# Optimization experiments

Measured on AMD Instinct MI355X. Metric: run time of the kernel, lower is better.

The kernel has to match this reference:

```python
import jax, jax.numpy as jnp
import numpy as np

B, S, D, V, T, NS, NG = 16, 512, 400, 32000, 8, 30, 3


def setup_inputs() -> dict:
    key = jax.random.key(0)
    ks = jax.random.split(key, 14)
    w = 1.0 / np.sqrt(D)
    return {
        "encoded_hidden": jax.random.normal(ks[0], (1, B, D), jnp.float32) * 0.1,
        "encoded_outputs": jax.random.normal(ks[1], (B, S, D), jnp.float32) * 0.1,
        "story": jax.random.randint(ks[2], (B, S), 0, V),
        "trg_batches": jax.random.randint(ks[3], (B, NS, T), 0, V),
        "shared_emb": jax.random.normal(ks[4], (V, D), jnp.float32) * 0.1,
        "slot_emb": jax.random.normal(ks[5], (1, D), jnp.float32) * 0.1,
        "w_ih": jax.random.normal(ks[6], (3 * D, D), jnp.float32) * w,
        "w_hh": jax.random.normal(ks[7], (3 * D, D), jnp.float32) * w,
        "b_ih": jax.random.normal(ks[8], (3 * D,), jnp.float32) * w,
        "b_hh": jax.random.normal(ks[9], (3 * D,), jnp.float32) * w,
        "w_ratio_w": jax.random.normal(ks[10], (1, 3 * D), jnp.float32) * w,
        "w_ratio_b": jax.random.normal(ks[11], (1,), jnp.float32) * w,
        "w_gate_w": jax.random.normal(ks[12], (NG, D), jnp.float32) * w,
        "w_gate_b": jax.random.normal(ks[13], (NG,), jnp.float32) * w,
        "batch_size": B,
        "max_resp_len": T,
    }


def reference(encoded_hidden, encoded_outputs, story, trg_batches, shared_emb,
              slot_emb, w_ih, w_hh, b_ih, b_hh, w_ratio_w, w_ratio_b,
              w_gate_w, w_gate_b, batch_size, max_resp_len):
    # Original torch code returns inside the slot loop -> only slot 0 is decoded.
    # h0 is re-used as GRU initial state at EVERY step (no carried hidden), and
    # teacher forcing makes each step's input known, so all T steps vectorize.
    h0 = encoded_hidden[0]                         # (B, D)
    Bq, Tq = batch_size, max_resp_len
    Vq = shared_emb.shape[0]

    # decoder inputs: step 0 = slot embedding, steps 1..T-1 = emb(trg[:,0,i-1])
    x0 = jnp.broadcast_to(slot_emb, h0.shape)      # (B, D)
    xt = shared_emb[trg_batches[:, 0, : Tq - 1]]   # (B, T-1, D)
    X = jnp.concatenate([x0[:, None, :], xt], axis=1)  # (B, T, D)

    # GRU cell (torch gate order r, z, n), h0 broadcast over steps
    gi = X @ w_ih.T + b_ih                         # (B, T, 3D)
    gh = h0 @ w_hh.T + b_hh                        # (B, 3D)
    i_r, i_z, i_n = jnp.split(gi, 3, axis=-1)
    h_r, h_z, h_n = jnp.split(gh, 3, axis=-1)
    r = jax.nn.sigmoid(i_r + h_r[:, None, :])
    z = jax.nn.sigmoid(i_z + h_z[:, None, :])
    n = jnp.tanh(i_n + r * h_n[:, None, :])
    h = (1.0 - z) * n + z * h0[:, None, :]         # (B, T, D) decoder_state == hidden

    # attention over history (no length masking: all lens == S)
    scores = jnp.einsum('btd,bsd->bts', h, encoded_outputs)   # (B, T, S)
    probs = jax.nn.softmax(scores, axis=-1)
    # FAITHFUL to original bug: context uses raw scores, not probs
    context = jnp.einsum('bts,bsd->btd', scores, encoded_outputs)

    gate0 = context[:, 0, :] @ w_gate_w.T + w_gate_b          # (B, NG), step i==0

    p_vocab = jax.nn.softmax(h @ shared_emb.T, axis=-1)       # (B, T, V)
    p_gen = jax.nn.sigmoid(
        jnp.concatenate([h, context, X], axis=-1) @ w_ratio_w.T + w_ratio_b
    )                                                         # (B, T, 1)

    # pointer distribution: scatter_add probs onto vocab ids of the story
    p_ctx = jnp.zeros((Bq, Tq, Vq), p_vocab.dtype).at[
        jnp.arange(Bq)[:, None, None],
        jnp.arange(Tq)[None, :, None],
        story[:, None, :],
    ].add(probs)

    p_final = p_gen * p_vocab + (1.0 - p_gen) * p_ctx         # (B, T, V)

    ptr_outputs = jnp.zeros((NS, Bq, Tq, Vq), p_final.dtype).at[0].set(p_final)
    gate_outputs = jnp.zeros((NS, Bq, NG), gate0.dtype).at[0].set(gate0)
    return ptr_outputs, gate_outputs
```

## Files before the change

kernel.cpp:

```cpp
#include <hip/hip_runtime.h>

#define Bq 16
#define Sq 512
#define Dq 400
#define Vq 32000
#define Tq 8
#define NSq 30
#define NGq 3
#define BTq (Bq*Tq)
#define SLICE 4096000
#define PTR_TOTAL (30ull*SLICE)
#define GATE_TOTAL (NSq*Bq*NGq)

#define NCOMPUTE 250
#define NZERO 1813
#define ZPER 16384

__device__ inline float sigmoidf_(float x) { return 1.0f / (1.0f + __expf(-x)); }

__device__ inline float blockReduceSum(float v, float* red) {
    int tid = threadIdx.x;
    #pragma unroll
    for (int o = 32; o > 0; o >>= 1) v += __shfl_down(v, o, 64);
    if ((tid & 63) == 0) red[tid >> 6] = v;
    __syncthreads();
    if (tid == 0) {
        float s = red[0];
        int nw = blockDim.x >> 6;
        for (int i = 1; i < nw; i++) s += red[i];
        red[0] = s;
    }
    __syncthreads();
    float r = red[0];
    __syncthreads();
    return r;
}

__device__ inline float blockReduceMax(float v, float* red) {
    int tid = threadIdx.x;
    #pragma unroll
    for (int o = 32; o > 0; o >>= 1) v = fmaxf(v, __shfl_down(v, o, 64));
    if ((tid & 63) == 0) red[tid >> 6] = v;
    __syncthreads();
    if (tid == 0) {
        float s = red[0];
        int nw = blockDim.x >> 6;
        for (int i = 1; i < nw; i++) s = fmaxf(s, red[i]);
        red[0] = s;
    }
    __syncthreads();
    float r = red[0];
    __syncthreads();
    return r;
}

__global__ __launch_bounds__(256) void k_gates(const float* __restrict__ enc_hidden,
                                               const float* __restrict__ shared_emb,
                                               const float* __restrict__ slot_emb,
                                               const float* __restrict__ w_ih,
                                               const float* __restrict__ w_hh,
                                               const float* __restrict__ b_ih,
                                               const float* __restrict__ b_hh,
                                               const int* __restrict__ trg,
                                               float* __restrict__ gi, float* __restrict__ gh) {
    __shared__ float A[9][Dq];
    __shared__ int toks[8];
    int b = blockIdx.x >> 2, jt = blockIdx.x & 3;
    int tid = threadIdx.x;
    if (tid < 7) toks[tid + 1] = trg[b * (NSq * Tq) + tid];
    __syncthreads();
    for (int idx = tid; idx < 900; idx += 256) {
        int r = idx / 100, q = idx - r * 100;
        const float4* src;
        if (r == 8)      src = (const float4*)(enc_hidden + b * Dq);
        else if (r == 0) src = (const float4*)slot_emb;
        else             src = (const float4*)(shared_emb + (size_t)toks[r] * Dq);
        *(float4*)&A[r][4 * q] = src[q];
    }
    __syncthreads();
    for (int o = tid; o < 2700; o += 256) {
        int r = o / 300, jj = o - r * 300;
        int j = jt * 300 + jj;
        const float* w = (r == 8) ? w_hh : w_ih;
        const float4* w4 = (const float4*)(w + (size_t)j * Dq);
        const float4* a4 = (const float4*)&A[r][0];
        float acc = (r == 8) ? b_hh[j] : b_ih[j];
        #pragma unroll 4
        for (int q = 0; q < Dq / 4; ++q) {
            float4 wv = w4[q], av = a4[q];
            acc += av.x * wv.x + av.y * wv.y + av.z * wv.z + av.w * wv.w;
        }
        if (r == 8) gh[b * 1200 + j] = acc;
        else        gi[(b * 8 + r) * 1200 + j] = acc;
    }
}

__global__ __launch_bounds__(512) void k_attn(const float* __restrict__ gi,
                                              const float* __restrict__ gh,
                                              const float* __restrict__ enc_hidden,
                                              const float* __restrict__ shared_emb,
                                              const float* __restrict__ slot_emb,
                                              const int* __restrict__ trg,
                                              const float* __restrict__ enc_out,
                                              const int* __restrict__ story,
                                              const float* __restrict__ w_ratio_w,
                                              const float* __restrict__ w_ratio_b,
                                              const float* __restrict__ w_gate_w,
                                              const float* __restrict__ w_gate_b,
                                              float* __restrict__ pctx, float* __restrict__ pgen,
                                              float* __restrict__ hT, float* __restrict__ out_gate) {
    __shared__ float h_l[Dq], ctx_l[Dq], x_l[Dq], sc_l[Sq], red[8];
    int bt = blockIdx.x, b = bt >> 3, t = bt & 7;
    int tid = threadIdx.x;
    if (tid < Dq) {
        int d = tid;
        float x = (t == 0) ? slot_emb[d]
                           : shared_emb[(size_t)trg[b * (NSq * Tq) + (t - 1)] * Dq + d];
        float h0 = enc_hidden[b * Dq + d];
        const float* gib = gi + bt * 1200;
        const float* ghb = gh + b * 1200;
        float r_ = sigmoidf_(gib[d] + ghb[d]);
        float z  = sigmoidf_(gib[Dq + d] + ghb[Dq + d]);
        float n  = tanhf(gib[2 * Dq + d] + r_ * ghb[2 * Dq + d]);
        float h  = (1.0f - z) * n + z * h0;
        h_l[d] = h; x_l[d] = x;
        hT[d * BTq + bt] = h;
    }
    __syncthreads();
    {
        const float4* e4 = (const float4*)(enc_out + ((size_t)(b * Sq + tid)) * Dq);
        float acc = 0.0f;
        for (int q = 0; q < Dq / 4; ++q) {
            float4 p = e4[q];
            int k = 4 * q;
            acc += h_l[k]*p.x + h_l[k+1]*p.y + h_l[k+2]*p.z + h_l[k+3]*p.w;
        }
        sc_l[tid] = acc;
    }
    __syncthreads();
    float myv = sc_l[tid];
    float m = blockReduceMax(myv, red);
    float e = __expf(myv - m);
    float ssum = blockReduceSum(e, red);
    atomicAdd(&pctx[(size_t)bt * Vq + story[b * Sq + tid]], e / ssum);
    for (int d = tid; d < Dq; d += 512) {
        float acc = 0.0f;
        #pragma unroll 8
        for (int s = 0; s < Sq; ++s)
            acc += sc_l[s] * enc_out[((size_t)(b * Sq + s)) * Dq + d];
        ctx_l[d] = acc;
    }
    __syncthreads();
    {
        float part = 0.0f;
        for (int i = tid; i < 1200; i += 512) {
            float v = (i < Dq) ? h_l[i] : (i < 2 * Dq ? ctx_l[i - Dq] : x_l[i - 2 * Dq]);
            part += v * w_ratio_w[i];
        }
        float tot = blockReduceSum(part, red);
        if (tid == 0) pgen[bt] = sigmoidf_(tot + w_ratio_b[0]);
    }
    if (t == 0) {
        for (int g = 0; g < NGq; ++g) {
            float part = 0.0f;
            for (int d = tid; d < Dq; d += 512) part += ctx_l[d] * w_gate_w[g * Dq + d];
            float tot = blockReduceSum(part, red);
            if (tid == 0) out_gate[b * NGq + g] = tot + w_gate_b[g];
        }
    }
}

#define TVL 128
#define CKL 40
__global__ __launch_bounds__(256) void k_logits(const float* __restrict__ hT,
                                                const float* __restrict__ emb,
                                                float* __restrict__ logits,
                                                float* __restrict__ out) {
    __shared__ float eT[CKL][132];
    __shared__ float hL[CKL][132];
    int bid = blockIdx.x;
    int tid = threadIdx.x;
    if (bid >= NCOMPUTE) {
        int zb = bid - NCOMPUTE;
        float4 z = make_float4(0.0f, 0.0f, 0.0f, 0.0f);
        if (zb < NZERO) {
            float4* dst = (float4*)(out + (size_t)SLICE);
            const size_t total = 29ull * SLICE / 4;
            size_t base = (size_t)zb * ZPER + tid;
            #pragma unroll
            for (int r = 0; r < ZPER / 256; ++r) {
                size_t idx = base + (size_t)r * 256;
                if (idx < total) dst[idx] = z;
            }
        } else {
            float4* g = (float4*)(out + PTR_TOTAL + Bq * NGq);
            for (int i = tid; i < (GATE_TOTAL - Bq * NGq) / 4; i += 256) g[i] = z;
        }
        return;
    }
    int v0 = bid * TVL;
    int tx = tid & 15, ty = tid >> 4;
    float acc[8][8];
    #pragma unroll
    for (int j = 0; j < 8; ++j)
        #pragma unroll
        for (int i = 0; i < 8; ++i) acc[j][i] = 0.0f;

    for (int c = 0; c < Dq / CKL; ++c) {
        int k0 = c * CKL;
        const float4* hg = (const float4*)(hT + (size_t)k0 * BTq);
        #pragma unroll
        for (int r = 0; r < 5; ++r) {
            int idx = tid + 256 * r;
            int k = idx >> 5, c4 = idx & 31;
            float4 vd = hg[idx];
            *(float4*)&hL[k][4 * c4] = vd;
        }
        #pragma unroll
        for (int r = 0; r < 5; ++r) {
            int idx = tid + 256 * r;
            int v = idx / 10, q = idx - 10 * v;
            float4 vd = *(const float4*)(emb + (size_t)(v0 + v) * Dq + k0 + 4 * q);
            eT[4*q+0][v] = vd.x; eT[4*q+1][v] = vd.y; eT[4*q+2][v] = vd.z; eT[4*q+3][v] = vd.w;
        }
        __syncthreads();
        #pragma unroll 4
        for (int k = 0; k < CKL; ++k) {
            float4 h0 = *(const float4*)&hL[k][8 * ty];
            float4 h1 = *(const float4*)&hL[k][8 * ty + 4];
            float4 e0 = *(const float4*)&eT[k][8 * tx];
            float4 e1 = *(const float4*)&eT[k][8 * tx + 4];
            float hv[8] = {h0.x, h0.y, h0.z, h0.w, h1.x, h1.y, h1.z, h1.w};
            float ev[8] = {e0.x, e0.y, e0.z, e0.w, e1.x, e1.y, e1.z, e1.w};
            #pragma unroll
            for (int j = 0; j < 8; ++j)
                #pragma unroll
                for (int i = 0; i < 8; ++i)
                    acc[j][i] += hv[j] * ev[i];
        }
        __syncthreads();
    }
    #pragma unroll
    for (int j = 0; j < 8; ++j) {
        int bt = 8 * ty + j;
        float* dst = logits + (size_t)bt * Vq + v0 + 8 * tx;
        *(float4*)dst       = make_float4(acc[j][0], acc[j][1], acc[j][2], acc[j][3]);
        *(float4*)(dst + 4) = make_float4(acc[j][4], acc[j][5], acc[j][6], acc[j][7]);
    }
}

__global__ __launch_bounds__(512) void k_final(const float* __restrict__ logits,
                                               const float* __restrict__ pctx,
                                               const float* __restrict__ pgen,
                                               float* __restrict__ out) {
    __shared__ float red[8];
    int bt = blockIdx.x, tid = threadIdx.x;
    const float* lr = logits + (size_t)bt * Vq;
    float m = -1e30f;
    for (int v = tid; v < Vq; v += 512) m = fmaxf(m, lr[v]);
    m = blockReduceMax(m, red);
    float s = 0.0f;
    for (int v = tid; v < Vq; v += 512) s += __expf(lr[v] - m);
    s = blockReduceSum(s, red);
    float inv = 1.0f / s, pg = pgen[bt], cg = 1.0f - pg;
    const float4* l4 = (const float4*)lr;
    const float4* p4 = (const float4*)(pctx + (size_t)bt * Vq);
    float4* o4 = (float4*)(out + (size_t)bt * Vq);
    for (int i = tid; i < Vq / 4; i += 512) {
        float4 lv = l4[i], pv = p4[i];
        o4[i] = make_float4(pg * __expf(lv.x - m) * inv + cg * pv.x,
                            pg * __expf(lv.y - m) * inv + cg * pv.y,
                            pg * __expf(lv.z - m) * inv + cg * pv.z,
                            pg * __expf(lv.w - m) * inv + cg * pv.w);
    }
}

extern "C" void kernel_launch(void* const* d_in, const int* in_sizes, int n_in,
                              void* d_out, int out_size, void* d_ws, size_t ws_size,
                              hipStream_t stream) {
    const float* enc_hidden = (const float*)d_in[0];
    const float* enc_out    = (const float*)d_in[1];
    const int*   story      = (const int*)d_in[2];
    const int*   trg        = (const int*)d_in[3];
    const float* shared_emb = (const float*)d_in[4];
    const float* slot_emb   = (const float*)d_in[5];
    const float* w_ih       = (const float*)d_in[6];
    const float* w_hh       = (const float*)d_in[7];
    const float* b_ih       = (const float*)d_in[8];
    const float* b_hh       = (const float*)d_in[9];
    const float* w_ratio_w  = (const float*)d_in[10];
    const float* w_ratio_b  = (const float*)d_in[11];
    const float* w_gate_w   = (const float*)d_in[12];
    const float* w_gate_b   = (const float*)d_in[13];

    float* out = (float*)d_out;

    float* ws = (float*)d_ws;
    float* logits_buf = ws;
    float* pctx_buf   = ws + (size_t)SLICE;
    float* gi_buf     = ws + 2 * (size_t)SLICE;
    float* gh_buf     = gi_buf + 153600;
    float* hT_buf     = gh_buf + 19200;
    float* pgen_buf   = hT_buf + 51200;

    hipMemsetAsync(pctx_buf, 0, (size_t)SLICE * sizeof(float), stream);

    hipLaunchKernelGGL(k_gates, dim3(64), dim3(256), 0, stream,
                       enc_hidden, shared_emb, slot_emb, w_ih, w_hh, b_ih, b_hh, trg,
                       gi_buf, gh_buf);
    hipLaunchKernelGGL(k_attn, dim3(BTq), dim3(512), 0, stream,
                       gi_buf, gh_buf, enc_hidden, shared_emb, slot_emb, trg,
                       enc_out, story, w_ratio_w, w_ratio_b, w_gate_w, w_gate_b,
                       pctx_buf, pgen_buf, hT_buf, out + PTR_TOTAL);
    hipLaunchKernelGGL(k_logits, dim3(NCOMPUTE + NZERO + 1), dim3(256), 0, stream,
                       hT_buf, shared_emb, logits_buf, out);
    hipLaunchKernelGGL(k_final, dim3(BTq), dim3(512), 0, stream,
                       logits_buf, pctx_buf, pgen_buf, out);
}
```

Before: 766.7 us.

## Spread output zero-fill across kernels and fold pctx memset into gates kernel

Removes the separate memset of the pointer-context buffer and instead zeroes it with extra blocks appended to the gates kernel. Splits the zero-filling of the 29 unused output slices between extra blocks in the attention kernel and the logits kernel, so the bandwidth-bound fill overlaps with the small, latency-bound compute kernels. The extra blocks may compete with the compute blocks for CUs and memory bandwidth. Launch sizes grow for the early kernels.

```diff
diff --git a/kernel.cpp b/kernel.cpp
--- a/kernel.cpp
+++ b/kernel.cpp
@@ -12,9 +12,12 @@
 #define PTR_TOTAL (30ull*SLICE)
 #define GATE_TOTAL (NSq*Bq*NGq)
 
+#define ZUNITS 1813
+#define ZPER 16384
+#define NZ_A 900
+#define NZ_B (ZUNITS - NZ_A)
 #define NCOMPUTE 250
-#define NZERO 1813
-#define ZPER 16384
+#define PCTX_ZB 63
 
 __device__ inline float sigmoidf_(float x) { return 1.0f / (1.0f + __expf(-x)); }
 
@@ -62,11 +65,26 @@
                                                const float* __restrict__ b_ih,
                                                const float* __restrict__ b_hh,
                                                const int* __restrict__ trg,
-                                               float* __restrict__ gi, float* __restrict__ gh) {
+                                               float* __restrict__ gi, float* __restrict__ gh,
+                                               float* __restrict__ pctx) {
     __shared__ float A[9][Dq];
     __shared__ int toks[8];
-    int b = blockIdx.x >> 2, jt = blockIdx.x & 3;
-    int tid = threadIdx.x;
+    int bid = blockIdx.x;
+    int tid = threadIdx.x;
+    if (bid >= 64) {
+        int zb = bid - 64;
+        const size_t total = (size_t)SLICE / 4;
+        float4 z = make_float4(0.0f, 0.0f, 0.0f, 0.0f);
+        float4* dst = (float4*)pctx;
+        size_t base = (size_t)zb * ZPER + tid;
+        #pragma unroll
+        for (int r = 0; r < ZPER / 256; ++r) {
+            size_t idx = base + (size_t)r * 256;
+            if (idx < total) dst[idx] = z;
+        }
+        return;
+    }
+    int b = bid >> 2, jt = bid & 3;
     if (tid < 7) toks[tid + 1] = trg[b * (NSq * Tq) + tid];
     __syncthreads();
     for (int idx = tid; idx < 900; idx += 256) {
@@ -108,10 +126,25 @@
                                               const float* __restrict__ w_gate_w,
                                               const float* __restrict__ w_gate_b,
                                               float* __restrict__ pctx, float* __restrict__ pgen,
-                                              float* __restrict__ hT, float* __restrict__ out_gate) {
+                                              float* __restrict__ hT, float* __restrict__ out_gate,
+                                              float* __restrict__ out) {
     __shared__ float h_l[Dq], ctx_l[Dq], x_l[Dq], sc_l[Sq], red[8];
-    int bt = blockIdx.x, b = bt >> 3, t = bt & 7;
-    int tid = threadIdx.x;
+    int bid = blockIdx.x;
+    int tid = threadIdx.x;
+    if (bid >= BTq) {
+        int zb = bid - BTq;
+        const size_t total = 29ull * SLICE / 4;
+        float4 z = make_float4(0.0f, 0.0f, 0.0f, 0.0f);
+        float4* dst = (float4*)(out + (size_t)SLICE);
+        size_t base = (size_t)zb * ZPER + tid;
+        #pragma unroll
+        for (int r = 0; r < ZPER / 512; ++r) {
+            size_t idx = base + (size_t)r * 512;
+            if (idx < total) dst[idx] = z;
+        }
+        return;
+    }
+    int bt = bid, b = bt >> 3, t = bt & 7;
     if (tid < Dq) {
         int d = tid;
         float x = (t == 0) ? slot_emb[d]
@@ -183,10 +216,11 @@
     if (bid >= NCOMPUTE) {
         int zb = bid - NCOMPUTE;
         float4 z = make_float4(0.0f, 0.0f, 0.0f, 0.0f);
-        if (zb < NZERO) {
+        if (zb < NZ_B) {
+            int unit = NZ_A + zb;
             float4* dst = (float4*)(out + (size_t)SLICE);
             const size_t total = 29ull * SLICE / 4;
-            size_t base = (size_t)zb * ZPER + tid;
+            size_t base = (size_t)unit * ZPER + tid;
             #pragma unroll
             for (int r = 0; r < ZPER / 256; ++r) {
                 size_t idx = base + (size_t)r * 256;
@@ -303,16 +337,14 @@
     float* hT_buf     = gh_buf + 19200;
     float* pgen_buf   = hT_buf + 51200;
 
-    hipMemsetAsync(pctx_buf, 0, (size_t)SLICE * sizeof(float), stream);
-
-    hipLaunchKernelGGL(k_gates, dim3(64), dim3(256), 0, stream,
+    hipLaunchKernelGGL(k_gates, dim3(64 + PCTX_ZB), dim3(256), 0, stream,
                        enc_hidden, shared_emb, slot_emb, w_ih, w_hh, b_ih, b_hh, trg,
-                       gi_buf, gh_buf);
-    hipLaunchKernelGGL(k_attn, dim3(BTq), dim3(512), 0, stream,
+                       gi_buf, gh_buf, pctx_buf);
+    hipLaunchKernelGGL(k_attn, dim3(BTq + NZ_A), dim3(512), 0, stream,
                        gi_buf, gh_buf, enc_hidden, shared_emb, slot_emb, trg,
                        enc_out, story, w_ratio_w, w_ratio_b, w_gate_w, w_gate_b,
-                       pctx_buf, pgen_buf, hT_buf, out + PTR_TOTAL);
-    hipLaunchKernelGGL(k_logits, dim3(NCOMPUTE + NZERO + 1), dim3(256), 0, stream,
+                       pctx_buf, pgen_buf, hT_buf, out + PTR_TOTAL, out);
+    hipLaunchKernelGGL(k_logits, dim3(NCOMPUTE + NZ_B + 1), dim3(256), 0, stream,
                        hT_buf, shared_emb, logits_buf, out);
     hipLaunchKernelGGL(k_final, dim3(BTq), dim3(512), 0, stream,
                        logits_buf, pctx_buf, pgen_buf, out);
```

Result: no change. 771.4 us (+0.6%).
